# Optimization experiments

Hardware: AMD Instinct MI355X
Metric: run time of the kernel (lower is better)

The kernel has to match this reference:

```python
import math
import jax, jax.numpy as jnp
import numpy as np

B, S, HID = 2, 1024, 1024
NH, HD = 16, 64
WIN = 4096
CACHE = 3072
EPS = 1e-5


def _clinear(xr, xi, Wr, Wi, br, bi):
    # complex linear: (xr + i xi)(Wr + i Wi)^T + (br + i bi)
    yr = xr @ Wr.T - xi @ Wi.T + br
    yi = xr @ Wi.T + xi @ Wr.T + bi
    return yr, yi


def _forward(hidden_re, hidden_im, K_cache_re, K_cache_im, V_cache_re, V_cache_im,
             gamma, beta_re, beta_im,
             q_Wr, q_Wi, q_br, q_bi, k_Wr, k_Wi, k_br, k_bi,
             v_Wr, v_Wi, v_br, v_bi, o_Wr, o_Wi, o_br, o_bi):
    batch, seq, _ = hidden_re.shape
    # --- complex LayerNorm: center complex mean, normalize by sqrt(E|x-mu|^2) ---
    mur = hidden_re.mean(-1, keepdims=True)
    mui = hidden_im.mean(-1, keepdims=True)
    cr = hidden_re - mur
    ci = hidden_im - mui
    inv = jax.lax.rsqrt((cr * cr + ci * ci).mean(-1, keepdims=True) + EPS)
    nr = cr * inv * gamma + beta_re
    ni = ci * inv * gamma + beta_im
    # --- projections ---
    Qr, Qi = _clinear(nr, ni, q_Wr, q_Wi, q_br, q_bi)
    Kr, Ki = _clinear(nr, ni, k_Wr, k_Wi, k_br, k_bi)
    Vr, Vi = _clinear(nr, ni, v_Wr, v_Wi, v_br, v_bi)
    Qr = Qr.reshape(batch, seq, NH, HD)
    Qi = Qi.reshape(batch, seq, NH, HD)
    Kr = Kr.reshape(batch, seq, NH, HD)
    Ki = Ki.reshape(batch, seq, NH, HD)
    Vr = Vr.reshape(batch, seq, NH, HD)
    Vi = Vi.reshape(batch, seq, NH, HD)
    # --- KV cache concat + window eviction (static shapes) ---
    cache_len = K_cache_re.shape[1]
    Kr = jnp.concatenate([K_cache_re, Kr], axis=1)
    Ki = jnp.concatenate([K_cache_im, Ki], axis=1)
    Vr = jnp.concatenate([V_cache_re, Vr], axis=1)
    Vi = jnp.concatenate([V_cache_im, Vi], axis=1)
    total_kv = Kr.shape[1]
    if total_kv > WIN:
        drop = total_kv - WIN
        Kr, Ki, Vr, Vi = Kr[:, drop:], Ki[:, drop:], Vr[:, drop:], Vi[:, drop:]
        cache_len = max(0, cache_len - drop)
        total_kv = WIN
    # --- Hermitian scores: Re(Q K^H) = Qr.Kr + Qi.Ki ---
    scale = 1.0 / math.sqrt(HD)
    scores = (jnp.einsum('bshd,bthd->bhst', Qr, Kr)
              + jnp.einsum('bshd,bthd->bhst', Qi, Ki)) * scale
    rows = jnp.arange(seq)[:, None]
    cols = jnp.arange(total_kv)[None, :]
    allowed = cols <= rows + cache_len  # causal within current chunk, full cache visible
    scores = jnp.where(allowed, scores, jnp.float32(-1e30))
    weights = jax.nn.softmax(scores, axis=-1)  # [B,NH,S,T]
    outr = jnp.einsum('bhst,bthd->bshd', weights, Vr).reshape(batch, seq, NH * HD)
    outi = jnp.einsum('bhst,bthd->bshd', weights, Vi).reshape(batch, seq, NH * HD)
    dr, di = _clinear(outr, outi, o_Wr, o_Wi, o_br, o_bi)
    out_re = hidden_re + dr
    out_im = hidden_im + di
    new_K_re, new_K_im = Kr[:, -WIN:], Ki[:, -WIN:]
    new_V_re, new_V_im = Vr[:, -WIN:], Vi[:, -WIN:]
    return out_re, out_im, new_K_re, new_K_im, new_V_re, new_V_im


def setup_inputs() -> dict:
    key = jax.random.key(0)
    ks = jax.random.split(key, 16)
    w = 0.02
    d = {
        'hidden_re': jax.random.normal(ks[0], (B, S, HID), jnp.float32),
        'hidden_im': jax.random.normal(ks[1], (B, S, HID), jnp.float32),
        'K_cache_re': jax.random.normal(ks[2], (B, CACHE, NH, HD), jnp.float32),
        'K_cache_im': jax.random.normal(ks[3], (B, CACHE, NH, HD), jnp.float32),
        'V_cache_re': jax.random.normal(ks[4], (B, CACHE, NH, HD), jnp.float32),
        'V_cache_im': jax.random.normal(ks[5], (B, CACHE, NH, HD), jnp.float32),
        'gamma': jnp.ones((HID,), jnp.float32),
        'beta_re': jnp.zeros((HID,), jnp.float32),
        'beta_im': jnp.zeros((HID,), jnp.float32),
    }
    for i, p in enumerate(['q', 'k', 'v', 'o']):
        d[p + '_Wr'] = jax.random.normal(ks[6 + 2 * i], (HID, HID), jnp.float32) * w
        d[p + '_Wi'] = jax.random.normal(ks[7 + 2 * i], (HID, HID), jnp.float32) * w
        d[p + '_br'] = jnp.zeros((HID,), jnp.float32)
        d[p + '_bi'] = jnp.zeros((HID,), jnp.float32)
    return d


def reference(hidden_re, hidden_im, K_cache_re, K_cache_im, V_cache_re, V_cache_im,
              gamma, beta_re, beta_im,
              q_Wr, q_Wi, q_br, q_bi, k_Wr, k_Wi, k_br, k_bi,
              v_Wr, v_Wi, v_br, v_bi, o_Wr, o_Wi, o_br, o_bi):
    return _forward(hidden_re, hidden_im, K_cache_re, K_cache_im, V_cache_re, V_cache_im,
                    gamma, beta_re, beta_im,
                    q_Wr, q_Wi, q_br, q_bi, k_Wr, k_Wi, k_br, k_bi,
                    v_Wr, v_Wi, v_br, v_bi, o_Wr, o_Wi, o_br, o_bi)
```

## Files before the change

### kernel.cpp

```cpp
#include <hip/hip_runtime.h>
#include <hip/hip_bf16.h>
#include <cstdint>
#include <cstddef>

typedef __bf16 bf16x8 __attribute__((ext_vector_type(8)));
typedef float  f32x4  __attribute__((ext_vector_type(4)));

__device__ __forceinline__ unsigned short f2bf(float f) {
  union { float f; unsigned u; } v; v.f = f;
  unsigned u = v.u;
  u += 0x7FFFu + ((u >> 16) & 1u);
  return (unsigned short)(u >> 16);
}

__device__ __forceinline__ unsigned short f2bf_cvt(float f) {
  __bf16 h = (__bf16)f;
  return __builtin_bit_cast(unsigned short, h);
}

__device__ __forceinline__ int imin(int a, int b) { return a < b ? a : b; }

struct alignas(16) US8 { unsigned short u[8]; };

__device__ __forceinline__ void g2lds16(const void* g, void* l) {
  __builtin_amdgcn_global_load_lds(
      (const __attribute__((address_space(1))) unsigned int*)g,
      (__attribute__((address_space(3))) unsigned int*)l, 16, 0, 0);
}

#define BB 2
#define SS 1024
#define HID 1024
#define NHH 16
#define HDD 64
#define TT 4096
#define CCH 3072
#define QSCALE (0.125f * 1.44269504088896f)

__global__ __launch_bounds__(256) void prep_kernel(
    const float* __restrict__ hre, const float* __restrict__ him,
    const float* __restrict__ gamma, const float* __restrict__ bre,
    const float* __restrict__ bim, unsigned short* __restrict__ Aln,
    const float* __restrict__ qWr, const float* __restrict__ qWi,
    const float* __restrict__ kWr, const float* __restrict__ kWi,
    const float* __restrict__ vWr, const float* __restrict__ vWi,
    const float* __restrict__ oWr, const float* __restrict__ oWi,
    unsigned short* __restrict__ Wc,
    const float* __restrict__ qbr, const float* __restrict__ qbi,
    const float* __restrict__ kbr, const float* __restrict__ kbi,
    const float* __restrict__ vbr, const float* __restrict__ vbi,
    const float* __restrict__ obr, const float* __restrict__ obi,
    float* __restrict__ bc)
{
  const int bid = blockIdx.x;
  const int tid = threadIdx.x;
  if (bid < 8192) {
    int gid = bid * 256 + tid;
    int idx = gid * 8;
    int p   = idx >> 22;
    int rem = idx & 0x3FFFFF;
    int n   = rem >> 11;
    int k   = rem & 2047;
    const float* Wr; const float* Wi;
    switch (p) {
      case 0:  Wr = qWr; Wi = qWi; break;
      case 1:  Wr = kWr; Wi = kWi; break;
      case 2:  Wr = vWr; Wi = vWi; break;
      default: Wr = oWr; Wi = oWi; break;
    }
    const float* src; float sgn = 1.f;
    if (n < 1024) {
      if (k < 1024) src = Wr + (size_t)n * 1024 + k;
      else        { src = Wi + (size_t)n * 1024 + (k - 1024); sgn = -1.f; }
    } else {
      if (k < 1024) src = Wi + (size_t)(n - 1024) * 1024 + k;
      else          src = Wr + (size_t)(n - 1024) * 1024 + (k - 1024);
    }
    float4 a = ((const float4*)src)[0];
    float4 b = ((const float4*)src)[1];
    US8 o;
    o.u[0] = f2bf(a.x * sgn); o.u[1] = f2bf(a.y * sgn);
    o.u[2] = f2bf(a.z * sgn); o.u[3] = f2bf(a.w * sgn);
    o.u[4] = f2bf(b.x * sgn); o.u[5] = f2bf(b.y * sgn);
    o.u[6] = f2bf(b.z * sgn); o.u[7] = f2bf(b.w * sgn);
    *(US8*)&Wc[idx] = o;
  } else if (bid < 10240) {
    int m = bid - 8192;
    const float4 vr = ((const float4*)(hre + (size_t)m * HID))[tid];
    const float4 vi = ((const float4*)(him + (size_t)m * HID))[tid];
    float sr = vr.x + vr.y + vr.z + vr.w;
    float si = vi.x + vi.y + vi.z + vi.w;
    float sq = vr.x*vr.x + vr.y*vr.y + vr.z*vr.z + vr.w*vr.w
             + vi.x*vi.x + vi.y*vi.y + vi.z*vi.z + vi.w*vi.w;
    __shared__ float red[3][4];
    int lane = tid & 63, w = tid >> 6;
    for (int off = 32; off; off >>= 1) {
      sr += __shfl_down(sr, off, 64);
      si += __shfl_down(si, off, 64);
      sq += __shfl_down(sq, off, 64);
    }
    if (lane == 0) { red[0][w] = sr; red[1][w] = si; red[2][w] = sq; }
    __syncthreads();
    sr = red[0][0] + red[0][1] + red[0][2] + red[0][3];
    si = red[1][0] + red[1][1] + red[1][2] + red[1][3];
    sq = red[2][0] + red[2][1] + red[2][2] + red[2][3];
    float mur = sr * (1.f/1024.f), mui = si * (1.f/1024.f);
    float var = sq * (1.f/1024.f) - mur*mur - mui*mui;
    float inv = rsqrtf(var + 1e-5f);
    int k = tid * 4;
    float4 g  = ((const float4*)gamma)[tid];
    float4 br = ((const float4*)bre)[tid];
    float4 bi = ((const float4*)bim)[tid];
    ushort4 nr, ni;
    nr.x = f2bf((vr.x - mur) * inv * g.x + br.x);
    nr.y = f2bf((vr.y - mur) * inv * g.y + br.y);
    nr.z = f2bf((vr.z - mur) * inv * g.z + br.z);
    nr.w = f2bf((vr.w - mur) * inv * g.w + br.w);
    ni.x = f2bf((vi.x - mui) * inv * g.x + bi.x);
    ni.y = f2bf((vi.y - mui) * inv * g.y + bi.y);
    ni.z = f2bf((vi.z - mui) * inv * g.z + bi.z);
    ni.w = f2bf((vi.w - mui) * inv * g.w + bi.w);
    *(ushort4*)&Aln[(size_t)m * 2048 + k]        = nr;
    *(ushort4*)&Aln[(size_t)m * 2048 + 1024 + k] = ni;
  } else {
    int idx = (bid - 10240) * 256 + tid;
    int p = idx >> 11, n = idx & 2047;
    const float* br; const float* bi;
    switch (p) {
      case 0:  br = qbr; bi = qbi; break;
      case 1:  br = kbr; bi = kbi; break;
      case 2:  br = vbr; bi = vbi; break;
      default: br = obr; bi = obi; break;
    }
    bc[idx] = (n < 1024) ? br[n] : bi[n - 1024];
  }
}

__global__ __launch_bounds__(256) void gemm_qkv_pack_kernel(
    const unsigned short* __restrict__ A, const unsigned short* __restrict__ Bm,
    const float* __restrict__ bias,
    unsigned short* __restrict__ Qp, unsigned short* __restrict__ Kp,
    float* __restrict__ out_Kre, float* __restrict__ out_Kim,
    float* __restrict__ out_Vre, float* __restrict__ out_Vim,
    const float* __restrict__ Kcr, const float* __restrict__ Kci)
{
  __shared__ alignas(16) unsigned short As[3][128][32];
  __shared__ alignas(16) unsigned short Bs[3][128][32];
  const int tid = threadIdx.x;
  if (blockIdx.x >= 768) {
    int pk = blockIdx.x - 768;
    int bh = pk / 384;
    int xx = pk % 384;
    int idx = (xx * 256 + tid) * 4;
    int d2 = idx & 127;
    int t  = idx >> 7;
    int b = bh >> 4, h = bh & 15;
    int d = d2 & 63;
    bool im = d2 >= 64;
    const float* src = im ? Kci : Kcr;
    float4 v = *(const float4*)&src[(((size_t)b * CCH + t) * 16 + h) * 64 + d];
    ushort4 o;
    o.x = f2bf(v.x); o.y = f2bf(v.y); o.z = f2bf(v.z); o.w = f2bf(v.w);
    *(ushort4*)&Kp[((size_t)bh * 4096 + t) * 128 + d2] = o;
    float* dst = im ? out_Kim : out_Kre;
    *(float4*)&dst[(((size_t)b * 4096 + t) * 16 + h) * 64 + d] = v;
    return;
  }
  const int K = 2048;
  const int NT = K / 32;
  int bm = (blockIdx.x / 48) * 128;
  int bn = (blockIdx.x % 48) * 128;
  int lane = tid & 63, w = tid >> 6;
  int wm = (w >> 1) * 64, wn = (w & 1) * 64;
  int l15 = lane & 15, q = lane >> 4;
  int lr = tid >> 2;
  int lcs = ((tid & 3) ^ ((tid >> 3) & 3)) * 8;

  const unsigned short* A0 = A  + (size_t)(bm + lr)      * K + lcs;
  const unsigned short* A1 = A  + (size_t)(bm + lr + 64) * K + lcs;
  const unsigned short* B0 = Bm + (size_t)(bn + lr)      * K + lcs;
  const unsigned short* B1 = Bm + (size_t)(bn + lr + 64) * K + lcs;
  const int rsw = ((l15 >> 1) & 3);

  f32x4 acc[4][4] = {};

  auto stage = [&](int b, int t) {
    int k0 = t * 32;
    g2lds16(A0 + k0, (unsigned short*)As[b] + 8*tid);
    g2lds16(A1 + k0, (unsigned short*)As[b] + 2048 + 8*tid);
    g2lds16(B0 + k0, (unsigned short*)Bs[b] + 8*tid);
    g2lds16(B1 + k0, (unsigned short*)Bs[b] + 2048 + 8*tid);
  };

  stage(0, 0);
  stage(1, 1);

  int bc_ = 0, bp_ = 2;
  for (int t = 0; t < NT; ++t) {
    if (t + 1 < NT) asm volatile("s_waitcnt vmcnt(4)" ::: "memory");
    else            asm volatile("s_waitcnt vmcnt(0)" ::: "memory");
    __builtin_amdgcn_s_barrier();
    __builtin_amdgcn_sched_barrier(0);
    if (t + 2 < NT) stage(bp_, t + 2);

    bf16x8 af[4], bfr[4];
#pragma unroll
    for (int i = 0; i < 4; i++) af[i]  = *(const bf16x8*)&As[bc_][wm + i*16 + l15][(q ^ rsw) * 8];
#pragma unroll
    for (int i = 0; i < 4; i++) bfr[i] = *(const bf16x8*)&Bs[bc_][wn + i*16 + l15][(q ^ rsw) * 8];
#pragma unroll
    for (int i = 0; i < 4; i++)
#pragma unroll
      for (int j = 0; j < 4; j++)
        acc[i][j] = __builtin_amdgcn_mfma_f32_16x16x32_bf16(af[i], bfr[j], acc[i][j], 0, 0, 0);

    bc_ = (bc_ == 2) ? 0 : bc_ + 1;
    bp_ = (bp_ == 2) ? 0 : bp_ + 1;
  }

  const int sec = bn >> 11;
#pragma unroll
  for (int i = 0; i < 4; i++)
#pragma unroll
    for (int j = 0; j < 4; j++) {
      int n = bn + wn + j*16 + l15;
      float bv = bias[n];
      int col = n & 2047;
      int re = (col < 1024) ? 1 : 0;
      int h = (col & 1023) >> 6, d = col & 63;
      int d2 = re ? d : 64 + d;
#pragma unroll
      for (int r = 0; r < 4; r++) {
        int m = bm + wm + i*16 + q*4 + r;
        float val = acc[i][j][r] + bv;
        int b = m >> 10, s = m & 1023;
        int bh = b*16 + h;
        if (sec == 0) {
          Qp[((size_t)bh*1024 + s)*128 + d2] = f2bf(val * QSCALE);
        } else if (sec == 1) {
          int t = CCH + s;
          Kp[((size_t)bh*4096 + t)*128 + d2] = f2bf(val);
          float* dst = re ? out_Kre : out_Kim;
          dst[(((size_t)b*4096 + t)*16 + h)*64 + d] = val;
        } else {
          int t = CCH + s;
          float* dst = re ? out_Vre : out_Vim;
          dst[(((size_t)b*4096 + t)*16 + h)*64 + d] = val;
        }
      }
    }
}

__global__ __launch_bounds__(256) void gemm_oproj_kernel(
    const unsigned short* __restrict__ A, const unsigned short* __restrict__ Bm,
    const float* __restrict__ bias, const float* __restrict__ hre,
    const float* __restrict__ him, float* __restrict__ out)
{
  __shared__ alignas(16) unsigned short As[3][128][32];
  __shared__ alignas(16) unsigned short Bs[3][128][32];
  const int K = 2048;
  const int NT = K / 32;
  int bm = blockIdx.y * 128;
  int bn = blockIdx.x * 128;
  int tid = threadIdx.x;
  int lane = tid & 63, w = tid >> 6;
  int wm = (w >> 1) * 64, wn = (w & 1) * 64;
  int l15 = lane & 15, q = lane >> 4;
  int lr = tid >> 2;
  int lcs = ((tid & 3) ^ ((tid >> 3) & 3)) * 8;

  const unsigned short* A0 = A  + (size_t)(bm + lr)      * K + lcs;
  const unsigned short* A1 = A  + (size_t)(bm + lr + 64) * K + lcs;
  const unsigned short* B0 = Bm + (size_t)(bn + lr)      * K + lcs;
  const unsigned short* B1 = Bm + (size_t)(bn + lr + 64) * K + lcs;
  const int rsw = ((l15 >> 1) & 3);

  f32x4 acc[4][4] = {};

  auto stage = [&](int b, int t) {
    int k0 = t * 32;
    g2lds16(A0 + k0, (unsigned short*)As[b] + 8*tid);
    g2lds16(A1 + k0, (unsigned short*)As[b] + 2048 + 8*tid);
    g2lds16(B0 + k0, (unsigned short*)Bs[b] + 8*tid);
    g2lds16(B1 + k0, (unsigned short*)Bs[b] + 2048 + 8*tid);
  };

  stage(0, 0);
  stage(1, 1);

  int bc_ = 0, bp_ = 2;
  for (int t = 0; t < NT; ++t) {
    if (t + 1 < NT) asm volatile("s_waitcnt vmcnt(4)" ::: "memory");
    else            asm volatile("s_waitcnt vmcnt(0)" ::: "memory");
    __builtin_amdgcn_s_barrier();
    __builtin_amdgcn_sched_barrier(0);
    if (t + 2 < NT) stage(bp_, t + 2);

    bf16x8 af[4], bfr[4];
#pragma unroll
    for (int i = 0; i < 4; i++) af[i]  = *(const bf16x8*)&As[bc_][wm + i*16 + l15][(q ^ rsw) * 8];
#pragma unroll
    for (int i = 0; i < 4; i++) bfr[i] = *(const bf16x8*)&Bs[bc_][wn + i*16 + l15][(q ^ rsw) * 8];
#pragma unroll
    for (int i = 0; i < 4; i++)
#pragma unroll
      for (int j = 0; j < 4; j++)
        acc[i][j] = __builtin_amdgcn_mfma_f32_16x16x32_bf16(af[i], bfr[j], acc[i][j], 0, 0, 0);

    bc_ = (bc_ == 2) ? 0 : bc_ + 1;
    bp_ = (bp_ == 2) ? 0 : bp_ + 1;
  }

#pragma unroll
  for (int i = 0; i < 4; i++)
#pragma unroll
    for (int j = 0; j < 4; j++) {
      int n = bn + wn + j*16 + l15;
      float bv = bias[n];
#pragma unroll
      for (int r = 0; r < 4; r++) {
        int m = bm + wm + i*16 + q*4 + r;
        float val = acc[i][j][r] + bv;
        if (n < 1024) out[(size_t)m * 1024 + n] = val + hre[(size_t)m * 1024 + n];
        else out[2097152 + (size_t)m * 1024 + (n - 1024)] = val + him[(size_t)m * 1024 + (n - 1024)];
      }
    }
}

__global__ __launch_bounds__(256) void pack_vt_fused_kernel(
    const float* __restrict__ Vc_re, const float* __restrict__ Vc_im,
    float* __restrict__ out_Vre, float* __restrict__ out_Vim,
    unsigned short* __restrict__ Vt)
{
  __shared__ float Ts[64][136];
  const int ty = blockIdx.x & 63;
  const int bh = blockIdx.x >> 6;
  const int b = bh >> 4, h = bh & 15;
  const int t0 = ty * 64;
  const int tid = threadIdx.x;
#pragma unroll
  for (int rr = 0; rr < 8; rr++) {
    int j = rr * 256 + tid;
    int t_loc = j >> 5, c = j & 31;
    int d2 = c * 4;
    int t = t0 + t_loc;
    int d = (d2 < 64) ? d2 : d2 - 64;
    float4 v;
    if (t < CCH) {
      const float* src = (d2 < 64) ? Vc_re : Vc_im;
      v = *(const float4*)&src[(((size_t)b * CCH + t) * 16 + h) * 64 + d];
      float* dst = (d2 < 64) ? out_Vre : out_Vim;
      *(float4*)&dst[(((size_t)b * 4096 + t) * 16 + h) * 64 + d] = v;
    } else {
      const float* src = (d2 < 64) ? out_Vre : out_Vim;
      v = *(const float4*)&src[(((size_t)b * 4096 + t) * 16 + h) * 64 + d];
    }
    *(float4*)&Ts[t_loc][d2] = v;
  }
  __syncthreads();
  const int d2 = tid >> 1, half = tid & 1;
  unsigned short tmp[32];
#pragma unroll
  for (int i = 0; i < 32; i++) tmp[i] = f2bf(Ts[half*32 + i][d2]);
  size_t dst = (size_t)bh * 128 * 4096 + (size_t)d2 * 4096 + t0 + half*32;
#pragma unroll
  for (int kq = 0; kq < 4; kq++)
    *(US8*)&Vt[dst + kq*8] = *(US8*)&tmp[kq*8];
}

__global__ __launch_bounds__(256) void attn_kernel(
    const unsigned short* __restrict__ Qp, const unsigned short* __restrict__ Kp,
    const unsigned short* __restrict__ Vt, float* __restrict__ Opart,
    float* __restrict__ Lpart)
{
  const int bh   = blockIdx.x;
  const int sblk = blockIdx.y;
  const int tpar = blockIdx.z;
  const int s0 = sblk * 128;
  const int tid = threadIdx.x;
  const int lane = tid & 63, w = tid >> 6;
  const int l15 = lane & 15, q = lane >> 4;

  __shared__ alignas(16) unsigned short Ks[3][32][128];
  __shared__ alignas(16) unsigned short Vs[2][128][32];
  __shared__ alignas(16) unsigned short Ps[4][32][40];

  bf16x8 qf[2][4];
#pragma unroll
  for (int mi = 0; mi < 2; mi++) {
    const size_t qb = ((size_t)bh * 1024 + s0 + w*32 + mi*16 + l15) * 128;
#pragma unroll
    for (int kc = 0; kc < 4; kc++)
      qf[mi][kc] = *(const bf16x8*)&Qp[qb + kc*32 + q*8];
  }

  f32x4 oacc[2][8] = {};
  float lsum[2][4] = {};

  const size_t kpb = (size_t)bh * 4096 * 128;
  const size_t vtb = (size_t)bh * 128 * 4096;
  const int n_tiles = 4*sblk + 100;
  const int n_safe  = n_tiles - 4;

  auto issueK = [&](int slot, int t0) {
#pragma unroll
    for (int kk = 0; kk < 2; kk++) {
      int j = (w*2 + kk)*64 + lane;
      int r = j >> 4, p = j & 15, c = p ^ (r & 7);
      g2lds16(&Kp[kpb + (size_t)(t0 + r) * 128 + c*8],
              (unsigned short*)&Ks[slot][0][0] + (size_t)j * 8);
    }
  };
  auto issueV = [&](int slot, int t0) {
#pragma unroll
    for (int kk = 0; kk < 2; kk++) {
      int j = (w*2 + kk)*64 + lane;
      int r = j >> 2, p = j & 3, c = p ^ ((r >> 1) & 3);
      g2lds16(&Vt[vtb + (size_t)r * 4096 + t0 + c*8],
              (unsigned short*)&Vs[slot][0][0] + (size_t)j * 8);
    }
  };

  const int t00 = tpar * 32;
  issueK(0, t00);
  issueK(1, imin((tpar + 3) * 32, 4064));
  issueV(0, t00);

  int kcur = 0, vcur = 0;
  for (int it = tpar; it < n_tiles; it += 3) {
    asm volatile("s_waitcnt vmcnt(4)" ::: "memory");
    __builtin_amdgcn_s_barrier();
    __builtin_amdgcn_sched_barrier(0);
    {
      int kslot = (kcur >= 1) ? kcur - 1 : kcur + 2;
      issueK(kslot, imin((it + 6) * 32, 4064));
      issueV(vcur ^ 1, imin((it + 3) * 32, 4064));
    }

    f32x4 sacc[2][2] = {};
    __builtin_amdgcn_s_setprio(1);
#pragma unroll
    for (int kc = 0; kc < 4; kc++) {
      bf16x8 kf[2];
#pragma unroll
      for (int nc = 0; nc < 2; nc++)
        kf[nc] = *(const bf16x8*)&Ks[kcur][nc*16 + l15][((kc*4 + q) ^ (l15 & 7)) * 8];
#pragma unroll
      for (int mi = 0; mi < 2; mi++)
#pragma unroll
        for (int nc = 0; nc < 2; nc++)
          sacc[mi][nc] = __builtin_amdgcn_mfma_f32_16x16x32_bf16(qf[mi][kc], kf[nc], sacc[mi][nc], 0, 0, 0);
    }
    __builtin_amdgcn_s_setprio(0);

    const bool safe = (it < n_safe);
    const int t0 = it << 5;
#pragma unroll
    for (int mi = 0; mi < 2; mi++)
#pragma unroll
      for (int r = 0; r < 4; r++) {
        const int rr = mi*16 + q*4 + r;
        const int rel = s0 + w*32 + rr + CCH - t0;
        float ls = 0.f;
#pragma unroll
        for (int nc = 0; nc < 2; nc++) {
          float p;
          asm("v_exp_f32 %0, %1" : "=v"(p) : "v"(sacc[mi][nc][r]));
          if (!safe && (nc*16 + l15 > rel)) p = 0.f;
          ls += p;
          Ps[w][rr][nc*16 + l15] = f2bf_cvt(p);
        }
        lsum[mi][r] += ls;
      }

    asm volatile("s_waitcnt vmcnt(4)" ::: "memory");
    __builtin_amdgcn_sched_barrier(0);

    bf16x8 pf[2];
#pragma unroll
    for (int mi = 0; mi < 2; mi++)
      pf[mi] = *(const bf16x8*)&Ps[w][mi*16 + l15][q*8];
    __builtin_amdgcn_s_setprio(1);
#pragma unroll
    for (int dc = 0; dc < 8; dc++) {
      int d2 = dc*16 + l15;
      bf16x8 vfr = *(const bf16x8*)&Vs[vcur][d2][(q ^ ((d2 >> 1) & 3)) * 8];
#pragma unroll
      for (int mi = 0; mi < 2; mi++)
        oacc[mi][dc] = __builtin_amdgcn_mfma_f32_16x16x32_bf16(pf[mi], vfr, oacc[mi][dc], 0, 0, 0);
    }
    __builtin_amdgcn_s_setprio(0);

    kcur = (kcur == 2) ? 0 : kcur + 1;
    vcur ^= 1;
  }

  asm volatile("s_waitcnt vmcnt(0)" ::: "memory");

  const size_t pb = ((size_t)tpar * 32 + bh) * 1024 + s0 + w*32;
#pragma unroll
  for (int mi = 0; mi < 2; mi++)
#pragma unroll
    for (int r = 0; r < 4; r++) {
      float l = lsum[mi][r];
      l += __shfl_xor(l, 1, 64);
      l += __shfl_xor(l, 2, 64);
      l += __shfl_xor(l, 4, 64);
      l += __shfl_xor(l, 8, 64);
      if (l15 == 0) Lpart[pb + mi*16 + q*4 + r] = l;
    }
#pragma unroll
  for (int mi = 0; mi < 2; mi++)
#pragma unroll
    for (int dc = 0; dc < 8; dc++)
#pragma unroll
      for (int r = 0; r < 4; r++)
        Opart[(pb + mi*16 + q*4 + r) * 128 + dc*16 + l15] = oacc[mi][dc][r];
}

__global__ __launch_bounds__(256) void attn_combine_kernel(
    const float* __restrict__ Opart, const float* __restrict__ Lpart,
    unsigned short* __restrict__ Ao)
{
  const size_t TS = 4194304ull;
  int gid = blockIdx.x * 256 + threadIdx.x;
  int idx = gid * 8;
  int m = idx >> 11, n0 = idx & 2047;
  int b = m >> 10, s = m & 1023;
  int h, d2_0;
  if (n0 < 1024) { h = n0 >> 6; d2_0 = n0 & 63; }
  else { h = (n0 - 1024) >> 6; d2_0 = 64 + ((n0 - 1024) & 63); }
  int bh = b*16 + h;
  size_t ob = ((size_t)bh * 1024 + s) * 128 + d2_0;
  float l0 = Lpart[(size_t)bh * 1024 + s];
  float l1 = Lpart[32768 + (size_t)bh * 1024 + s];
  float l2 = Lpart[65536 + (size_t)bh * 1024 + s];
  float inv = 1.f / (l0 + l1 + l2);
  float4 x0 = *(const float4*)&Opart[ob];
  float4 x1 = *(const float4*)&Opart[ob + 4];
  float4 y0 = *(const float4*)&Opart[ob + TS];
  float4 y1 = *(const float4*)&Opart[ob + TS + 4];
  float4 z0 = *(const float4*)&Opart[ob + 2*TS];
  float4 z1 = *(const float4*)&Opart[ob + 2*TS + 4];
  US8 o;
  o.u[0] = f2bf((x0.x + y0.x + z0.x) * inv); o.u[1] = f2bf((x0.y + y0.y + z0.y) * inv);
  o.u[2] = f2bf((x0.z + y0.z + z0.z) * inv); o.u[3] = f2bf((x0.w + y0.w + z0.w) * inv);
  o.u[4] = f2bf((x1.x + y1.x + z1.x) * inv); o.u[5] = f2bf((x1.y + y1.y + z1.y) * inv);
  o.u[6] = f2bf((x1.z + y1.z + z1.z) * inv); o.u[7] = f2bf((x1.w + y1.w + z1.w) * inv);
  *(US8*)&Ao[idx] = o;
}

extern "C" void kernel_launch(void* const* d_in, const int* in_sizes, int n_in,
                              void* d_out, int out_size, void* d_ws, size_t ws_size,
                              hipStream_t stream)
{
  (void)in_sizes; (void)n_in; (void)out_size; (void)ws_size;
  const float* hre = (const float*)d_in[0];
  const float* him = (const float*)d_in[1];
  const float* Kcr = (const float*)d_in[2];
  const float* Kci = (const float*)d_in[3];
  const float* Vcr = (const float*)d_in[4];
  const float* Vci = (const float*)d_in[5];
  const float* gamma = (const float*)d_in[6];
  const float* bre = (const float*)d_in[7];
  const float* bim = (const float*)d_in[8];
  const float* qWr = (const float*)d_in[9];
  const float* qWi = (const float*)d_in[10];
  const float* qbr = (const float*)d_in[11];
  const float* qbi = (const float*)d_in[12];
  const float* kWr = (const float*)d_in[13];
  const float* kWi = (const float*)d_in[14];
  const float* kbr = (const float*)d_in[15];
  const float* kbi = (const float*)d_in[16];
  const float* vWr = (const float*)d_in[17];
  const float* vWi = (const float*)d_in[18];
  const float* vbr = (const float*)d_in[19];
  const float* vbi = (const float*)d_in[20];
  const float* oWr = (const float*)d_in[21];
  const float* oWi = (const float*)d_in[22];
  const float* obr = (const float*)d_in[23];
  const float* obi = (const float*)d_in[24];
  float* out = (float*)d_out;

  char* ws = (char*)d_ws;
  size_t off = 0;
  auto carve = [&](size_t bytes) {
    char* p = ws + off;
    off += (bytes + 255) & ~(size_t)255;
    return p;
  };
  unsigned short* Aln  = (unsigned short*)carve(2048ull * 2048 * 2);
  unsigned short* Wc   = (unsigned short*)carve(4ull * 2048 * 2048 * 2);
  float*          bc   = (float*)carve(4ull * 2048 * 4);
  unsigned short* Qp   = (unsigned short*)carve(4194304ull * 2);
  unsigned short* Kp   = (unsigned short*)carve(16777216ull * 2);
  unsigned short* Vt   = (unsigned short*)carve(16777216ull * 2);
  float*          Opart= (float*)carve(3ull * 32 * 1024 * 128 * 4);
  float*          Lpart= (float*)carve(3ull * 32 * 1024 * 4);

  unsigned short* Ao = Aln;

  float* out_Kre = out + 4194304;
  float* out_Kim = out + 4194304 + 8388608;
  float* out_Vre = out + 4194304 + 2 * 8388608;
  float* out_Vim = out + 4194304 + 3 * 8388608;

  hipLaunchKernelGGL(prep_kernel, dim3(10272), dim3(256), 0, stream,
                     hre, him, gamma, bre, bim, Aln,
                     qWr, qWi, kWr, kWi, vWr, vWi, oWr, oWi, Wc,
                     qbr, qbi, kbr, kbi, vbr, vbi, obr, obi, bc);
  hipLaunchKernelGGL(gemm_qkv_pack_kernel, dim3(13056), dim3(256), 0, stream,
                     Aln, Wc, bc, Qp, Kp, out_Kre, out_Kim, out_Vre, out_Vim,
                     Kcr, Kci);
  hipLaunchKernelGGL(pack_vt_fused_kernel, dim3(2048), dim3(256), 0, stream,
                     Vcr, Vci, out_Vre, out_Vim, Vt);
  hipLaunchKernelGGL(attn_kernel, dim3(32, 8, 3), dim3(256), 0, stream,
                     Qp, Kp, Vt, Opart, Lpart);
  hipLaunchKernelGGL(attn_combine_kernel, dim3(2048), dim3(256), 0, stream,
                     Opart, Lpart, Ao);
  hipLaunchKernelGGL(gemm_oproj_kernel, dim3(16, 16), dim3(256), 0, stream,
                     Ao, Wc + 3ull * 2048 * 2048, bc + 3 * 2048, hre, him, out);
}
```

Baseline: 571.2 us.

## Widen QKV GEMM tile to 128x256 and simplify attention K/V double buffering

The QKV projection GEMM now uses 512-thread blocks with a 128x256 output tile, so each A tile is loaded once for twice as many columns; the cache-packing tail blocks are rescaled to match. The bf16 conversion in its epilogue switches to the hardware cast. The attention kernel replaces its three-slot K / two-slot V prefetch, which used explicit vmcnt waits, with a plain double buffer guarded by __syncthreads. The larger tile reduces global traffic per output but raises LDS use and register pressure, and the simpler attention pipeline prefetches less far ahead, so load latency may be less hidden.

```diff
diff --git a/kernel.cpp b/kernel.cpp
--- a/kernel.cpp
+++ b/kernel.cpp
@@ -17,8 +17,6 @@
   __bf16 h = (__bf16)f;
   return __builtin_bit_cast(unsigned short, h);
 }
-
-__device__ __forceinline__ int imin(int a, int b) { return a < b ? a : b; }
 
 struct alignas(16) US8 { unsigned short u[8]; };
 
@@ -136,7 +134,7 @@
   }
 }
 
-__global__ __launch_bounds__(256) void gemm_qkv_pack_kernel(
+__global__ __launch_bounds__(512) void gemm_qkv_pack_kernel(
     const unsigned short* __restrict__ A, const unsigned short* __restrict__ Bm,
     const float* __restrict__ bias,
     unsigned short* __restrict__ Qp, unsigned short* __restrict__ Kp,
@@ -145,13 +143,13 @@
     const float* __restrict__ Kcr, const float* __restrict__ Kci)
 {
   __shared__ alignas(16) unsigned short As[3][128][32];
-  __shared__ alignas(16) unsigned short Bs[3][128][32];
+  __shared__ alignas(16) unsigned short Bs[3][256][32];
   const int tid = threadIdx.x;
-  if (blockIdx.x >= 768) {
-    int pk = blockIdx.x - 768;
-    int bh = pk / 384;
-    int xx = pk % 384;
-    int idx = (xx * 256 + tid) * 4;
+  if (blockIdx.x >= 384) {
+    int pk = blockIdx.x - 384;
+    int bh = pk / 192;
+    int xx = pk % 192;
+    int idx = (xx * 512 + tid) * 4;
     int d2 = idx & 127;
     int t  = idx >> 7;
     int b = bh >> 4, h = bh & 15;
@@ -168,28 +166,26 @@
   }
   const int K = 2048;
   const int NT = K / 32;
-  int bm = (blockIdx.x / 48) * 128;
-  int bn = (blockIdx.x % 48) * 128;
+  int bm = (blockIdx.x / 24) * 128;
+  int bn = (blockIdx.x % 24) * 256;
   int lane = tid & 63, w = tid >> 6;
-  int wm = (w >> 1) * 64, wn = (w & 1) * 64;
+  int wm = (w >> 2) * 64, wn = (w & 3) * 64;
   int l15 = lane & 15, q = lane >> 4;
   int lr = tid >> 2;
   int lcs = ((tid & 3) ^ ((tid >> 3) & 3)) * 8;
 
-  const unsigned short* A0 = A  + (size_t)(bm + lr)      * K + lcs;
-  const unsigned short* A1 = A  + (size_t)(bm + lr + 64) * K + lcs;
-  const unsigned short* B0 = Bm + (size_t)(bn + lr)      * K + lcs;
-  const unsigned short* B1 = Bm + (size_t)(bn + lr + 64) * K + lcs;
+  const unsigned short* Ag  = A  + (size_t)(bm + lr)       * K + lcs;
+  const unsigned short* Bg0 = Bm + (size_t)(bn + lr)       * K + lcs;
+  const unsigned short* Bg1 = Bm + (size_t)(bn + lr + 128) * K + lcs;
   const int rsw = ((l15 >> 1) & 3);
 
   f32x4 acc[4][4] = {};
 
   auto stage = [&](int b, int t) {
     int k0 = t * 32;
-    g2lds16(A0 + k0, (unsigned short*)As[b] + 8*tid);
-    g2lds16(A1 + k0, (unsigned short*)As[b] + 2048 + 8*tid);
-    g2lds16(B0 + k0, (unsigned short*)Bs[b] + 8*tid);
-    g2lds16(B1 + k0, (unsigned short*)Bs[b] + 2048 + 8*tid);
+    g2lds16(Ag  + k0, (unsigned short*)As[b] + 8*tid);
+    g2lds16(Bg0 + k0, (unsigned short*)Bs[b] + 8*tid);
+    g2lds16(Bg1 + k0, (unsigned short*)Bs[b] + 4096 + 8*tid);
   };
 
   stage(0, 0);
@@ -197,7 +193,7 @@
 
   int bc_ = 0, bp_ = 2;
   for (int t = 0; t < NT; ++t) {
-    if (t + 1 < NT) asm volatile("s_waitcnt vmcnt(4)" ::: "memory");
+    if (t + 1 < NT) asm volatile("s_waitcnt vmcnt(3)" ::: "memory");
     else            asm volatile("s_waitcnt vmcnt(0)" ::: "memory");
     __builtin_amdgcn_s_barrier();
     __builtin_amdgcn_sched_barrier(0);
@@ -236,10 +232,10 @@
         int b = m >> 10, s = m & 1023;
         int bh = b*16 + h;
         if (sec == 0) {
-          Qp[((size_t)bh*1024 + s)*128 + d2] = f2bf(val * QSCALE);
+          Qp[((size_t)bh*1024 + s)*128 + d2] = f2bf_cvt(val * QSCALE);
         } else if (sec == 1) {
           int t = CCH + s;
-          Kp[((size_t)bh*4096 + t)*128 + d2] = f2bf(val);
+          Kp[((size_t)bh*4096 + t)*128 + d2] = f2bf_cvt(val);
           float* dst = re ? out_Kre : out_Kim;
           dst[(((size_t)b*4096 + t)*16 + h)*64 + d] = val;
         } else {
@@ -381,7 +377,7 @@
   const int lane = tid & 63, w = tid >> 6;
   const int l15 = lane & 15, q = lane >> 4;
 
-  __shared__ alignas(16) unsigned short Ks[3][32][128];
+  __shared__ alignas(16) unsigned short Ks[2][32][128];
   __shared__ alignas(16) unsigned short Vs[2][128][32];
   __shared__ alignas(16) unsigned short Ps[4][32][40];
 
@@ -402,40 +398,29 @@
   const int n_tiles = 4*sblk + 100;
   const int n_safe  = n_tiles - 4;
 
-  auto issueK = [&](int slot, int t0) {
+  auto issue = [&](int buf, int t0) {
 #pragma unroll
     for (int kk = 0; kk < 2; kk++) {
       int j = (w*2 + kk)*64 + lane;
       int r = j >> 4, p = j & 15, c = p ^ (r & 7);
       g2lds16(&Kp[kpb + (size_t)(t0 + r) * 128 + c*8],
-              (unsigned short*)&Ks[slot][0][0] + (size_t)j * 8);
-    }
-  };
-  auto issueV = [&](int slot, int t0) {
+              (unsigned short*)&Ks[buf][0][0] + (size_t)j * 8);
+    }
 #pragma unroll
     for (int kk = 0; kk < 2; kk++) {
       int j = (w*2 + kk)*64 + lane;
       int r = j >> 2, p = j & 3, c = p ^ ((r >> 1) & 3);
       g2lds16(&Vt[vtb + (size_t)r * 4096 + t0 + c*8],
-              (unsigned short*)&Vs[slot][0][0] + (size_t)j * 8);
+              (unsigned short*)&Vs[buf][0][0] + (size_t)j * 8);
     }
   };
 
-  const int t00 = tpar * 32;
-  issueK(0, t00);
-  issueK(1, imin((tpar + 3) * 32, 4064));
-  issueV(0, t00);
-
-  int kcur = 0, vcur = 0;
+  int buf = 0;
+  issue(0, tpar * 32);
+
   for (int it = tpar; it < n_tiles; it += 3) {
-    asm volatile("s_waitcnt vmcnt(4)" ::: "memory");
-    __builtin_amdgcn_s_barrier();
-    __builtin_amdgcn_sched_barrier(0);
-    {
-      int kslot = (kcur >= 1) ? kcur - 1 : kcur + 2;
-      issueK(kslot, imin((it + 6) * 32, 4064));
-      issueV(vcur ^ 1, imin((it + 3) * 32, 4064));
-    }
+    __syncthreads();
+    if (it + 3 < n_tiles) issue(buf ^ 1, (it + 3) * 32);
 
     f32x4 sacc[2][2] = {};
     __builtin_amdgcn_s_setprio(1);
@@ -444,7 +429,7 @@
       bf16x8 kf[2];
 #pragma unroll
       for (int nc = 0; nc < 2; nc++)
-        kf[nc] = *(const bf16x8*)&Ks[kcur][nc*16 + l15][((kc*4 + q) ^ (l15 & 7)) * 8];
+        kf[nc] = *(const bf16x8*)&Ks[buf][nc*16 + l15][((kc*4 + q) ^ (l15 & 7)) * 8];
 #pragma unroll
       for (int mi = 0; mi < 2; mi++)
 #pragma unroll
@@ -473,9 +458,6 @@
         lsum[mi][r] += ls;
       }
 
-    asm volatile("s_waitcnt vmcnt(4)" ::: "memory");
-    __builtin_amdgcn_sched_barrier(0);
-
     bf16x8 pf[2];
 #pragma unroll
     for (int mi = 0; mi < 2; mi++)
@@ -484,18 +466,14 @@
 #pragma unroll
     for (int dc = 0; dc < 8; dc++) {
       int d2 = dc*16 + l15;
-      bf16x8 vfr = *(const bf16x8*)&Vs[vcur][d2][(q ^ ((d2 >> 1) & 3)) * 8];
+      bf16x8 vfr = *(const bf16x8*)&Vs[buf][d2][(q ^ ((d2 >> 1) & 3)) * 8];
 #pragma unroll
       for (int mi = 0; mi < 2; mi++)
         oacc[mi][dc] = __builtin_amdgcn_mfma_f32_16x16x32_bf16(pf[mi], vfr, oacc[mi][dc], 0, 0, 0);
     }
     __builtin_amdgcn_s_setprio(0);
-
-    kcur = (kcur == 2) ? 0 : kcur + 1;
-    vcur ^= 1;
+    buf ^= 1;
   }
-
-  asm volatile("s_waitcnt vmcnt(0)" ::: "memory");
 
   const size_t pb = ((size_t)tpar * 32 + bh) * 1024 + s0 + w*32;
 #pragma unroll
@@ -609,7 +587,7 @@
                      hre, him, gamma, bre, bim, Aln,
                      qWr, qWi, kWr, kWi, vWr, vWi, oWr, oWi, Wc,
                      qbr, qbi, kbr, kbi, vbr, vbi, obr, obi, bc);
-  hipLaunchKernelGGL(gemm_qkv_pack_kernel, dim3(13056), dim3(256), 0, stream,
+  hipLaunchKernelGGL(gemm_qkv_pack_kernel, dim3(6528), dim3(512), 0, stream,
                      Aln, Wc, bc, Qp, Kp, out_Kre, out_Kim, out_Vre, out_Vim,
                      Kcr, Kci);
   hipLaunchKernelGGL(pack_vt_fused_kernel, dim3(2048), dim3(256), 0, stream,
```

New measurement: 553.7 us. -3.1%, faster.
